# Optimization experiments

Measured on AMD Instinct MI355X. Metric: run time of the kernel, lower is better.

Reference implementation:

```python
import jax, jax.numpy as jnp
import numpy as np

B, H, D, SIZE, S = 32, 16, 64, 262144, 1024
GAMMA = 0.99

def setup_inputs() -> dict:
    key = jax.random.key(0)
    k1, k2, k3, k4 = jax.random.split(key, 4)
    return {
        "query": jax.random.normal(k1, (B, H, D), jnp.float32),
        "key_store": jax.random.normal(k2, (SIZE, H, D), jnp.float32),
        "value_store": jax.random.normal(k3, (SIZE, H, D), jnp.float32),
        "logit_store": 0.1 * jax.random.normal(k4, (SIZE, H), jnp.float32),
    }

def _sample_indices(logit_store, batch, rng):
    # torch softmax over dim=0 (batch*head rows) => per-row weights over s are
    # w[s] proportional to exp(logit[s,h]) / sum_h' exp(logit[s,h'])
    logw = logit_store.T - jax.nn.logsumexp(logit_store, axis=1)[None, :]  # (H, SIZE)
    u = jax.random.uniform(rng, (batch,) + logw.shape, minval=1e-12, maxval=1.0)
    gumbel = -jnp.log(-jnp.log(u))
    # Gumbel top-k == sampling without replacement proportional to exp(logw)
    _, idx = jax.lax.top_k(logw[None] + gumbel, S)  # (B, H, S)
    return idx

def reference(query, key_store, value_store, logit_store):
    b, h, d = query.shape
    idx = _sample_indices(logit_store, b, jax.random.key(42))  # (B,H,S)
    hidx = jnp.arange(h)[None, :, None]  # (1,H,1) broadcasts against idx
    kst = key_store.transpose(1, 0, 2)   # (H, SIZE, D)
    vst = value_store.transpose(1, 0, 2)
    sk = kst[hidx, idx]  # (B,H,S,D) gathered sample keys
    sv = vst[hidx, idx]  # (B,H,S,D) gathered sample values
    attn = jax.nn.softmax(jnp.einsum('bhd,bhsd->bhs', query, sk) * (d ** -0.5), axis=-1)
    lerp_k = jnp.einsum('bhs,bhsd->bhd', attn, sk)
    lerp_v = jnp.einsum('bhs,bhsd->bhd', attn, sv)
    # scattered in-place store updates
    new_k = (1.0 - attn)[..., None] * sk + attn[..., None] * lerp_k[:, :, None, :]
    new_v = (1.0 - attn)[..., None] * sv + attn[..., None] * lerp_v[:, :, None, :]
    key_store_new = kst.at[hidx, idx].set(new_k).transpose(1, 0, 2)
    value_store_new = vst.at[hidx, idx].set(new_v).transpose(1, 0, 2)
    lst = logit_store.T  # (H, SIZE)
    new_l = GAMMA * lst[hidx, idx] + attn  # RHS uses gathered old logits (matches torch)
    logit_store_new = lst.at[hidx, idx].set(new_l).T
    return lerp_k, lerp_v, key_store_new, value_store_new, logit_store_new
```

## Files before the change

### kernel.cpp

```cpp
#include <hip/hip_runtime.h>
#include <stdint.h>

static constexpr int NB = 32, NH = 16, ND = 64, NS = 1024;
static constexpr int SZ = 262144;
static constexpr int NROW = NB * NH;
static constexpr long N4 = 67108864L;
static constexpr long SPLIT4 = 50331648L;
static constexpr int SPLIT_IDX = 196608;

typedef float f32x4 __attribute__((ext_vector_type(4)));

__device__ __forceinline__ uint32_t rotl32(uint32_t x, int r) { return (x << r) | (x >> (32 - r)); }

__device__ __forceinline__ void tf2x32(uint32_t x0, uint32_t x1, uint32_t& o0, uint32_t& o1) {
  const uint32_t K1 = 42u, K2 = 0x1BD11BF0u;
  x1 += K1;
#define TFR(r) { x0 += x1; x1 = rotl32(x1, (r)); x1 ^= x0; }
  TFR(13) TFR(15) TFR(26) TFR(6)
  x0 += K1; x1 += K2 + 1u;
  TFR(17) TFR(29) TFR(16) TFR(24)
  x0 += K2; x1 += 2u;
  TFR(13) TFR(15) TFR(26) TFR(6)
  x1 += K1 + 3u;
  TFR(17) TFR(29) TFR(16) TFR(24)
  x0 += K1; x1 += K2 + 4u;
  TFR(13) TFR(15) TFR(26) TFR(6)
  x0 += K2; x1 += 5u;
#undef TFR
  o0 = x0; o1 = x1;
}

__device__ __forceinline__ uint32_t bits_of(uint32_t row, uint32_t s) {
  uint32_t o0, o1; tf2x32(0u, (row << 18) | s, o0, o1);
  return o0 ^ o1;
}

__device__ __forceinline__ float gumbel_precise(uint32_t row, uint32_t s) {
  uint32_t bits = bits_of(row, s);
  float f = __uint_as_float((bits >> 9) | 0x3f800000u) - 1.0f;
  float u = fmaxf(1e-12f, f + 1e-12f);
  float t = -logf(u);
  return -logf(t);
}

__device__ __forceinline__ float uf_of(uint32_t row, uint32_t s) {
  return __uint_as_float((bits_of(row, s) >> 9) | 0x3f800000u);
}

__device__ __forceinline__ uint32_t fkey(float v) {
  uint32_t u = __float_as_uint(v);
  return (u & 0x80000000u) ? ~u : (u | 0x80000000u);
}

__global__ void k_logw(const float* __restrict__ logit, float* __restrict__ logw,
                       float* __restrict__ wexp, float* __restrict__ outL,
                       int* __restrict__ winner, float* __restrict__ W) {
  __shared__ float sW[16];
  const int tid = threadIdx.x;
  if (tid < 16) sW[tid] = 0.f;
  __syncthreads();
  int s = blockIdx.x * 256 + tid;
  const float4* p = (const float4*)(logit + (size_t)s * NH);
  float4 a0 = p[0], a1 = p[1], a2 = p[2], a3 = p[3];
  float x[16] = {a0.x,a0.y,a0.z,a0.w, a1.x,a1.y,a1.z,a1.w,
                 a2.x,a2.y,a2.z,a2.w, a3.x,a3.y,a3.z,a3.w};
  float m = x[0];
#pragma unroll
  for (int h = 1; h < 16; ++h) m = fmaxf(m, x[h]);
  float acc = 0.f;
#pragma unroll
  for (int h = 0; h < 16; ++h) acc += expf(x[h] - m);
  float lse = logf(acc) + m;
  float wl[16];
#pragma unroll
  for (int h = 0; h < 16; ++h) {
    float lw = x[h] - lse;
    logw[(size_t)h * SZ + s] = lw;
    float e = expf(lw);
    wexp[(size_t)h * SZ + s] = e;
    wl[h] = e;
  }
#pragma unroll
  for (int h = 0; h < 16; ++h) {
    float v = wl[h];
#pragma unroll
    for (int off = 32; off; off >>= 1) v += __shfl_xor(v, off);
    if ((tid & 63) == 0) atomicAdd(&sW[h], v);
  }
  float4* q = (float4*)(outL + (size_t)s * NH);
  q[0] = a0; q[1] = a1; q[2] = a2; q[3] = a3;
  int4 mone = make_int4(-1, -1, -1, -1);
  int4* w = (int4*)(winner + (size_t)s * NH);
  w[0] = mone; w[1] = mone; w[2] = mone; w[3] = mone;
  __syncthreads();
  if (tid < 16) atomicAdd(&W[tid], sW[tid]);
}

__device__ __forceinline__ void find_thresh(const uint32_t* hist, int nbins, int chunk,
                                            uint32_t need, int* outT, int tid) {
  if (tid < 64) {
    int hi = nbins - 1 - tid * chunk;
    uint32_t csum = 0;
    for (int j = 0; j < chunk; ++j) csum += hist[hi - j];
    uint32_t inc = csum;
#pragma unroll
    for (int off = 1; off < 64; off <<= 1) {
      uint32_t t = (uint32_t)__shfl_up((int)inc, off);
      if (tid >= off) inc += t;
    }
    uint32_t pre = inc - csum;
    if (pre < need && inc >= need) {
      uint32_t cum = pre; int T = hi - chunk + 1;
      for (int j = 0; j < chunk; ++j) {
        int b = hi - j;
        if (cum + hist[b] >= need) { T = b; break; }
        cum += hist[b];
      }
      *outT = T;
    }
  }
}

#define MEGA_T 512
#define SEL_BLKS 512
#define COPY_BLKS 2048
#define NCAND 5120
__global__ void __launch_bounds__(MEGA_T, 8) k_mega(
    const float* __restrict__ logw, const float* __restrict__ wexp,
    const float* __restrict__ Wsum, const float* __restrict__ qin,
    const float* __restrict__ Kst, const float* __restrict__ Vst,
    int* __restrict__ idx_sel, float* __restrict__ attn_ws,
    float* __restrict__ lerp_k, float* __restrict__ lerp_v, int* __restrict__ winner,
    f32x4* __restrict__ oK4, f32x4* __restrict__ oV4) {
  const int bid = blockIdx.x;
  const int tid = threadIdx.x;

  if (bid >= SEL_BLKS) {
    const f32x4* K4 = (const f32x4*)Kst;
    const f32x4* V4 = (const f32x4*)Vst;
    const long base = (long)(bid - SEL_BLKS) * MEGA_T + tid;
    const long stride = (long)COPY_BLKS * MEGA_T;
    for (int r = 0; r < 12; ++r) {
      long i0 = base + (long)(4 * r) * stride;
      long i1 = i0 + stride, i2 = i0 + 2 * stride, i3 = i0 + 3 * stride;
      f32x4 k0 = __builtin_nontemporal_load(&K4[i0]);
      f32x4 k1 = __builtin_nontemporal_load(&K4[i1]);
      f32x4 k2 = __builtin_nontemporal_load(&K4[i2]);
      f32x4 k3 = __builtin_nontemporal_load(&K4[i3]);
      f32x4 v0 = __builtin_nontemporal_load(&V4[i0]);
      f32x4 v1 = __builtin_nontemporal_load(&V4[i1]);
      f32x4 v2 = __builtin_nontemporal_load(&V4[i2]);
      f32x4 v3 = __builtin_nontemporal_load(&V4[i3]);
      __builtin_nontemporal_store(k0, &oK4[i0]);
      __builtin_nontemporal_store(k1, &oK4[i1]);
      __builtin_nontemporal_store(k2, &oK4[i2]);
      __builtin_nontemporal_store(k3, &oK4[i3]);
      __builtin_nontemporal_store(v0, &oV4[i0]);
      __builtin_nontemporal_store(v1, &oV4[i1]);
      __builtin_nontemporal_store(v2, &oV4[i2]);
      __builtin_nontemporal_store(v3, &oV4[i3]);
    }
    return;
  }

  const int row = bid;
  const int h = row & 15, b = row >> 4;
  const float* lw = logw + (size_t)h * SZ;
  const f32x4* we4 = (const f32x4*)(wexp + (size_t)h * SZ);
  int* outrow = idx_sel + (size_t)row * NS;

  __shared__ union {
    struct {
      int      cidx[NCAND];
      uint32_t hist[2048];
      uint16_t candA[2048];
      uint16_t candB[256];
      uint16_t candC[64];
    } s;
    struct {
      int   sel_s[NS];
      float sc[NS];
      float red[MEGA_T];
      f32x4 pk4[8][16], pv4[8][16];
    } a;
  } u;
  __shared__ int ctl[8];
  __shared__ float sNB;

  if (tid == 0) {
    float Wh = Wsum[h];
    sNB = -4096.0f / Wh;
    ctl[1] = 0;
  }
  __syncthreads();
  const float nB = sNB;
  const float CThr = 1.9999996f;

  for (int g = tid; g < SZ / 4; g += MEGA_T) {
    f32x4 w4 = we4[g];
    int s0 = g << 2;
    float u0 = uf_of(row, s0);
    float u1 = uf_of(row, s0 + 1);
    float u2 = uf_of(row, s0 + 2);
    float u3 = uf_of(row, s0 + 3);
    if (u0 >= fmaf(nB, w4.x, CThr)) { int p = atomicAdd(&ctl[1], 1); if (p < NCAND) u.s.cidx[p] = s0; }
    if (u1 >= fmaf(nB, w4.y, CThr)) { int p = atomicAdd(&ctl[1], 1); if (p < NCAND) u.s.cidx[p] = s0 + 1; }
    if (u2 >= fmaf(nB, w4.z, CThr)) { int p = atomicAdd(&ctl[1], 1); if (p < NCAND) u.s.cidx[p] = s0 + 2; }
    if (u3 >= fmaf(nB, w4.w, CThr)) { int p = atomicAdd(&ctl[1], 1); if (p < NCAND) u.s.cidx[p] = s0 + 3; }
  }
  __syncthreads();
  const int C = min(ctl[1], NCAND);

  for (int i = tid; i < 2048; i += MEGA_T) u.s.hist[i] = 0;
  if (tid == 0) { ctl[0] = 0; ctl[3] = 0; ctl[4] = 0; ctl[5] = 0; }
  __syncthreads();
  for (int ci = tid; ci < C; ci += MEGA_T) {
    int s = u.s.cidx[ci];
    uint32_t k = fkey(lw[s] + gumbel_precise(row, s));
    atomicAdd(&u.s.hist[k >> 21], 1u);
  }
  __syncthreads();
  find_thresh(u.s.hist, 2048, 32, (uint32_t)NS, &ctl[2], tid);
  __syncthreads();
  const int T0 = ctl[2];
  for (int ci = tid; ci < C; ci += MEGA_T) {
    int s = u.s.cidx[ci];
    uint32_t k = fkey(lw[s] + gumbel_precise(row, s));
    int bb = (int)(k >> 21);
    if (bb > T0)       { int p = atomicAdd(&ctl[0], 1); outrow[p] = s; }
    else if (bb == T0) { int c = atomicAdd(&ctl[3], 1); if (c < 2048) u.s.candA[c] = (uint16_t)ci; }
  }
  __syncthreads();
  const int CA = min(ctl[3], 2048);
  for (int i = tid; i < 2048; i += MEGA_T) u.s.hist[i] = 0;
  __syncthreads();
  for (int i = tid; i < CA; i += MEGA_T) {
    int s = u.s.cidx[u.s.candA[i]];
    uint32_t k = fkey(lw[s] + gumbel_precise(row, s));
    atomicAdd(&u.s.hist[(k >> 10) & 0x7FFu], 1u);
  }
  __syncthreads();
  find_thresh(u.s.hist, 2048, 32, (uint32_t)(NS - ctl[0]), &ctl[2], tid);
  __syncthreads();
  const int T1 = ctl[2];
  for (int i = tid; i < CA; i += MEGA_T) {
    int ci = u.s.candA[i];
    int s = u.s.cidx[ci];
    uint32_t k = fkey(lw[s] + gumbel_precise(row, s));
    int mid = (int)((k >> 10) & 0x7FFu);
    if (mid > T1)       { int p = atomicAdd(&ctl[0], 1); outrow[p] = s; }
    else if (mid == T1) { int c = atomicAdd(&ctl[4], 1); if (c < 256) u.s.candB[c] = (uint16_t)ci; }
  }
  __syncthreads();
  const int CB = min(ctl[4], 256);
  for (int i = tid; i < 1024; i += MEGA_T) u.s.hist[i] = 0;
  __syncthreads();
  for (int i = tid; i < CB; i += MEGA_T) {
    int s = u.s.cidx[u.s.candB[i]];
    uint32_t k = fkey(lw[s] + gumbel_precise(row, s));
    atomicAdd(&u.s.hist[k & 0x3FFu], 1u);
  }
  __syncthreads();
  find_thresh(u.s.hist, 1024, 16, (uint32_t)(NS - ctl[0]), &ctl[2], tid);
  __syncthreads();
  const int T2 = ctl[2];
  for (int i = tid; i < CB; i += MEGA_T) {
    int ci = u.s.candB[i];
    int s = u.s.cidx[ci];
    uint32_t k = fkey(lw[s] + gumbel_precise(row, s));
    int lo = (int)(k & 0x3FFu);
    if (lo > T2)       { int p = atomicAdd(&ctl[0], 1); outrow[p] = s; }
    else if (lo == T2) { int c = atomicAdd(&ctl[5], 1); if (c < 64) u.s.candC[c] = (uint16_t)ci; }
  }
  __syncthreads();
  if (tid == 0) {
    int need = NS - ctl[0];
    int cc = min(ctl[5], 64);
    for (int k = 0; k < need; ++k) {
      int best = 0x7fffffff, bi = 0;
      for (int j = 0; j < cc; ++j) { int s = u.s.cidx[u.s.candC[j]]; if (s < best) { best = s; bi = j; } }
      if (best == 0x7fffffff) best = 0;
      outrow[ctl[0] + k] = best;
      if (cc > 0) u.s.cidx[u.s.candC[bi]] = 0x7fffffff;
    }
  }
  __syncthreads();

  const f32x4* K4 = (const f32x4*)Kst;
  const f32x4* V4 = (const f32x4*)Vst;
  const int lane = tid & 63, wv = tid >> 6;
  const int sj = lane >> 3, dj = lane & 7;
  for (int i = tid; i < NS; i += MEGA_T) u.a.sel_s[i] = outrow[i];
  const f32x4* q4 = (const f32x4*)(qin + (size_t)row * ND);
  f32x4 qa = q4[dj * 2], qb = q4[dj * 2 + 1];
  __syncthreads();
  for (int it = 0; it < 16; it += 2) {
    int i1 = it * 64 + wv * 8 + sj;
    int i2 = i1 + 64;
    int x1 = u.a.sel_s[i1], x2 = u.a.sel_s[i2];
    size_t b1 = ((size_t)x1 * NH + h) * 16 + dj * 2;
    size_t b2 = ((size_t)x2 * NH + h) * 16 + dj * 2;
    f32x4 ka1 = K4[b1], kb1 = K4[b1 + 1];
    f32x4 ka2 = K4[b2], kb2 = K4[b2 + 1];
    float p1 = ka1.x*qa.x + ka1.y*qa.y + ka1.z*qa.z + ka1.w*qa.w
             + kb1.x*qb.x + kb1.y*qb.y + kb1.z*qb.z + kb1.w*qb.w;
    float p2 = ka2.x*qa.x + ka2.y*qa.y + ka2.z*qa.z + ka2.w*qa.w
             + kb2.x*qb.x + kb2.y*qb.y + kb2.z*qb.z + kb2.w*qb.w;
#pragma unroll
    for (int off = 1; off < 8; off <<= 1) { p1 += __shfl_xor(p1, off); p2 += __shfl_xor(p2, off); }
    if (dj == 0) { u.a.sc[i1] = p1 * 0.125f; u.a.sc[i2] = p2 * 0.125f; }
  }
  __syncthreads();
  float v1 = u.a.sc[tid], v2 = u.a.sc[tid + 512];
  u.a.red[tid] = fmaxf(v1, v2); __syncthreads();
  for (int s = 256; s; s >>= 1) { if (tid < s) u.a.red[tid] = fmaxf(u.a.red[tid], u.a.red[tid + s]); __syncthreads(); }
  float m = u.a.red[0]; __syncthreads();
  float e1 = expf(v1 - m), e2 = expf(v2 - m);
  u.a.red[tid] = e1 + e2; __syncthreads();
  for (int s = 256; s; s >>= 1) { if (tid < s) u.a.red[tid] += u.a.red[tid + s]; __syncthreads(); }
  float inv = 1.0f / u.a.red[0];
  float a1 = e1 * inv, a2 = e2 * inv;
  u.a.sc[tid] = a1; u.a.sc[tid + 512] = a2;
  attn_ws[(size_t)row * NS + tid] = a1;
  attn_ws[(size_t)row * NS + tid + 512] = a2;
  __syncthreads();
  f32x4 AK = 0.f, BK = 0.f, AV = 0.f, BV = 0.f;
  for (int it = 0; it < 16; it += 2) {
    int i1 = it * 64 + wv * 8 + sj;
    int i2 = i1 + 64;
    int x1 = u.a.sel_s[i1], x2 = u.a.sel_s[i2];
    float c1 = u.a.sc[i1], c2 = u.a.sc[i2];
    size_t b1 = ((size_t)x1 * NH + h) * 16 + dj * 2;
    size_t b2 = ((size_t)x2 * NH + h) * 16 + dj * 2;
    f32x4 k1a = K4[b1], k1b = K4[b1 + 1], v1a = V4[b1], v1b = V4[b1 + 1];
    f32x4 k2a = K4[b2], k2b = K4[b2 + 1], v2a = V4[b2], v2b = V4[b2 + 1];
    AK += c1 * k1a + c2 * k2a; BK += c1 * k1b + c2 * k2b;
    AV += c1 * v1a + c2 * v2a; BV += c1 * v1b + c2 * v2b;
  }
#pragma unroll
  for (int off = 8; off < 64; off <<= 1) {
    AK.x += __shfl_xor(AK.x, off); AK.y += __shfl_xor(AK.y, off);
    AK.z += __shfl_xor(AK.z, off); AK.w += __shfl_xor(AK.w, off);
    BK.x += __shfl_xor(BK.x, off); BK.y += __shfl_xor(BK.y, off);
    BK.z += __shfl_xor(BK.z, off); BK.w += __shfl_xor(BK.w, off);
    AV.x += __shfl_xor(AV.x, off); AV.y += __shfl_xor(AV.y, off);
    AV.z += __shfl_xor(AV.z, off); AV.w += __shfl_xor(AV.w, off);
    BV.x += __shfl_xor(BV.x, off); BV.y += __shfl_xor(BV.y, off);
    BV.w += __shfl_xor(BV.w, off); BV.z += __shfl_xor(BV.z, off);
  }
  if (sj == 0) {
    u.a.pk4[wv][dj * 2] = AK; u.a.pk4[wv][dj * 2 + 1] = BK;
    u.a.pv4[wv][dj * 2] = AV; u.a.pv4[wv][dj * 2 + 1] = BV;
  }
  __syncthreads();
  if (tid < 64) {
    float lk = 0.f, lv = 0.f;
    const float* pkf = (const float*)u.a.pk4;
    const float* pvf = (const float*)u.a.pv4;
#pragma unroll
    for (int ww = 0; ww < 8; ++ww) { lk += pkf[ww * 64 + tid]; lv += pvf[ww * 64 + tid]; }
    lerp_k[(size_t)row * ND + tid] = lk;
    lerp_v[(size_t)row * ND + tid] = lv;
  }
  for (int i = tid; i < NS; i += MEGA_T) atomicMax(&winner[(size_t)u.a.sel_s[i] * NH + h], b);
}

__global__ void k_mark(const int* __restrict__ idx_sel, const float* __restrict__ attn_ws,
                       const int* __restrict__ winner, const float* __restrict__ Lst,
                       float* __restrict__ wa, float* __restrict__ outL) {
  int t = blockIdx.x * 256 + threadIdx.x;
  int row = t >> 10, h = row & 15, b = row >> 4;
  int idx = idx_sel[t];
  size_t slot = (size_t)idx * NH + h;
  if (winner[slot] == b) {
    float a = attn_ws[t];
    wa[slot] = a;
    outL[slot] = 0.99f * Lst[slot] + a;
  }
}

__global__ void __launch_bounds__(512) k_emit2(const f32x4* __restrict__ K4,
    const f32x4* __restrict__ V4, const int* __restrict__ winner,
    const float* __restrict__ wa, const f32x4* __restrict__ LK4,
    const f32x4* __restrict__ LV4, f32x4* __restrict__ oK4, f32x4* __restrict__ oV4) {
  const long base = SPLIT4 + (long)blockIdx.x * 512 + threadIdx.x;
  const long stride = 2048L * 512;
  for (int r = 0; r < 4; ++r) {
    long i0 = base + (long)(4 * r) * stride;
    long i1 = i0 + stride, i2 = i0 + 2 * stride, i3 = i0 + 3 * stride;
    int s0 = (int)(i0 >> 4), s1 = (int)(i1 >> 4), s2 = (int)(i2 >> 4), s3 = (int)(i3 >> 4);
    int w0 = winner[s0], w1 = winner[s1], w2 = winner[s2], w3 = winner[s3];
    f32x4 k0 = __builtin_nontemporal_load(&K4[i0]);
    f32x4 k1 = __builtin_nontemporal_load(&K4[i1]);
    f32x4 k2 = __builtin_nontemporal_load(&K4[i2]);
    f32x4 k3 = __builtin_nontemporal_load(&K4[i3]);
    f32x4 v0 = __builtin_nontemporal_load(&V4[i0]);
    f32x4 v1 = __builtin_nontemporal_load(&V4[i1]);
    f32x4 v2 = __builtin_nontemporal_load(&V4[i2]);
    f32x4 v3 = __builtin_nontemporal_load(&V4[i3]);
    if (w0 >= 0) {
      float a = wa[s0]; int rr = (w0 << 4) | (s0 & 15); float o = 1.0f - a;
      k0 = o * k0 + a * LK4[((long)rr << 4) + (i0 & 15)];
      v0 = o * v0 + a * LV4[((long)rr << 4) + (i0 & 15)];
    }
    if (w1 >= 0) {
      float a = wa[s1]; int rr = (w1 << 4) | (s1 & 15); float o = 1.0f - a;
      k1 = o * k1 + a * LK4[((long)rr << 4) + (i1 & 15)];
      v1 = o * v1 + a * LV4[((long)rr << 4) + (i1 & 15)];
    }
    if (w2 >= 0) {
      float a = wa[s2]; int rr = (w2 << 4) | (s2 & 15); float o = 1.0f - a;
      k2 = o * k2 + a * LK4[((long)rr << 4) + (i2 & 15)];
      v2 = o * v2 + a * LV4[((long)rr << 4) + (i2 & 15)];
    }
    if (w3 >= 0) {
      float a = wa[s3]; int rr = (w3 << 4) | (s3 & 15); float o = 1.0f - a;
      k3 = o * k3 + a * LK4[((long)rr << 4) + (i3 & 15)];
      v3 = o * v3 + a * LV4[((long)rr << 4) + (i3 & 15)];
    }
    __builtin_nontemporal_store(k0, &oK4[i0]);
    __builtin_nontemporal_store(k1, &oK4[i1]);
    __builtin_nontemporal_store(k2, &oK4[i2]);
    __builtin_nontemporal_store(k3, &oK4[i3]);
    __builtin_nontemporal_store(v0, &oV4[i0]);
    __builtin_nontemporal_store(v1, &oV4[i1]);
    __builtin_nontemporal_store(v2, &oV4[i2]);
    __builtin_nontemporal_store(v3, &oV4[i3]);
  }
}

__global__ void __launch_bounds__(256) k_fixup(const float* __restrict__ Kst,
    const float* __restrict__ Vst, const int* __restrict__ idx_sel,
    const float* __restrict__ attn_ws, const int* __restrict__ winner,
    const float* __restrict__ lerp_k, const float* __restrict__ lerp_v,
    float* __restrict__ outK, float* __restrict__ outV) {
  int g = blockIdx.x * 4 + (threadIdx.x >> 6);
  int lane = threadIdx.x & 63;
  int row = g >> 10, i = g & 1023;
  int h = row & 15, b = row >> 4;
  int idx = idx_sel[(size_t)row * NS + i];
  if (idx >= SPLIT_IDX) return;
  size_t slot = (size_t)idx * NH + h;
  if (winner[slot] != b) return;
  float a = attn_ws[(size_t)row * NS + i];
  size_t base = slot * ND + lane;
  float kv = Kst[base], vv = Vst[base];
  float lk = lerp_k[(size_t)row * ND + lane], lv = lerp_v[(size_t)row * ND + lane];
  float o = 1.0f - a;
  outK[base] = o * kv + a * lk;
  outV[base] = o * vv + a * lv;
}

extern "C" void kernel_launch(void* const* d_in, const int* in_sizes, int n_in,
                              void* d_out, int out_size, void* d_ws, size_t ws_size,
                              hipStream_t stream) {
  const float* q   = (const float*)d_in[0];
  const float* Kst = (const float*)d_in[1];
  const float* Vst = (const float*)d_in[2];
  const float* Lst = (const float*)d_in[3];

  float* out    = (float*)d_out;
  float* out_lk = out;
  float* out_lv = out + 32768;
  float* outK   = out + 65536;
  float* outV   = outK + 268435456;
  float* outL   = outV + 268435456;

  char* ws = (char*)d_ws;
  float* logw   = (float*)ws;
  float* wexp   = (float*)(ws + (16ull << 20));
  int*   idxsel = (int*)(ws + (32ull << 20));
  float* attn   = (float*)(ws + (34ull << 20));
  int*   winner = (int*)(ws + (36ull << 20));
  float* wa     = (float*)(ws + (52ull << 20));
  float* Wsum   = (float*)(ws + (68ull << 20));

  hipMemsetAsync(Wsum, 0, 16 * sizeof(float), stream);
  k_logw<<<SZ / 256, 256, 0, stream>>>(Lst, logw, wexp, outL, winner, Wsum);
  k_mega<<<SEL_BLKS + COPY_BLKS, MEGA_T, 0, stream>>>(logw, wexp, Wsum, q, Kst, Vst,
                                                      idxsel, attn, out_lk, out_lv, winner,
                                                      (f32x4*)outK, (f32x4*)outV);
  k_mark<<<NROW * NS / 256, 256, 0, stream>>>(idxsel, attn, winner, Lst, wa, outL);
  k_emit2<<<2048, 512, 0, stream>>>((const f32x4*)Kst, (const f32x4*)Vst, winner, wa,
                                    (const f32x4*)out_lk, (const f32x4*)out_lv,
                                    (f32x4*)outK, (f32x4*)outV);
  k_fixup<<<NROW * NS / 4, 256, 0, stream>>>(Kst, Vst, idxsel, attn, winner,
                                             out_lk, out_lv, outK, outV);
}
```

Baseline: 1.173 ms.

## Split store copy evenly and fuse emit and fixup into one tail kernel

```diff
diff --git a/kernel.cpp b/kernel.cpp
--- a/kernel.cpp
+++ b/kernel.cpp
@@ -5,8 +5,8 @@
 static constexpr int SZ = 262144;
 static constexpr int NROW = NB * NH;
 static constexpr long N4 = 67108864L;
-static constexpr long SPLIT4 = 50331648L;
-static constexpr int SPLIT_IDX = 196608;
+static constexpr long HALF4 = 33554432L;
+static constexpr int SPLIT_IDX = 131072;
 
 typedef float f32x4 __attribute__((ext_vector_type(4)));
 
@@ -140,7 +140,7 @@
     const f32x4* V4 = (const f32x4*)Vst;
     const long base = (long)(bid - SEL_BLKS) * MEGA_T + tid;
     const long stride = (long)COPY_BLKS * MEGA_T;
-    for (int r = 0; r < 12; ++r) {
+    for (int r = 0; r < 8; ++r) {
       long i0 = base + (long)(4 * r) * stride;
       long i1 = i0 + stride, i2 = i0 + 2 * stride, i3 = i0 + 3 * stride;
       f32x4 k0 = __builtin_nontemporal_load(&K4[i0]);
@@ -346,7 +346,7 @@
     AV.x += __shfl_xor(AV.x, off); AV.y += __shfl_xor(AV.y, off);
     AV.z += __shfl_xor(AV.z, off); AV.w += __shfl_xor(AV.w, off);
     BV.x += __shfl_xor(BV.x, off); BV.y += __shfl_xor(BV.y, off);
-    BV.w += __shfl_xor(BV.w, off); BV.z += __shfl_xor(BV.z, off);
+    BV.z += __shfl_xor(BV.z, off); BV.w += __shfl_xor(BV.w, off);
   }
   if (sj == 0) {
     u.a.pk4[wv][dj * 2] = AK; u.a.pk4[wv][dj * 2 + 1] = BK;
@@ -379,62 +379,61 @@
   }
 }
 
-__global__ void __launch_bounds__(512) k_emit2(const f32x4* __restrict__ K4,
+#define TAIL_COPY_BLKS 4096
+__global__ void __launch_bounds__(256) k_tail(const f32x4* __restrict__ K4,
     const f32x4* __restrict__ V4, const int* __restrict__ winner,
     const float* __restrict__ wa, const f32x4* __restrict__ LK4,
-    const f32x4* __restrict__ LV4, f32x4* __restrict__ oK4, f32x4* __restrict__ oV4) {
-  const long base = SPLIT4 + (long)blockIdx.x * 512 + threadIdx.x;
-  const long stride = 2048L * 512;
-  for (int r = 0; r < 4; ++r) {
-    long i0 = base + (long)(4 * r) * stride;
-    long i1 = i0 + stride, i2 = i0 + 2 * stride, i3 = i0 + 3 * stride;
-    int s0 = (int)(i0 >> 4), s1 = (int)(i1 >> 4), s2 = (int)(i2 >> 4), s3 = (int)(i3 >> 4);
-    int w0 = winner[s0], w1 = winner[s1], w2 = winner[s2], w3 = winner[s3];
-    f32x4 k0 = __builtin_nontemporal_load(&K4[i0]);
-    f32x4 k1 = __builtin_nontemporal_load(&K4[i1]);
-    f32x4 k2 = __builtin_nontemporal_load(&K4[i2]);
-    f32x4 k3 = __builtin_nontemporal_load(&K4[i3]);
-    f32x4 v0 = __builtin_nontemporal_load(&V4[i0]);
-    f32x4 v1 = __builtin_nontemporal_load(&V4[i1]);
-    f32x4 v2 = __builtin_nontemporal_load(&V4[i2]);
-    f32x4 v3 = __builtin_nontemporal_load(&V4[i3]);
-    if (w0 >= 0) {
-      float a = wa[s0]; int rr = (w0 << 4) | (s0 & 15); float o = 1.0f - a;
-      k0 = o * k0 + a * LK4[((long)rr << 4) + (i0 & 15)];
-      v0 = o * v0 + a * LV4[((long)rr << 4) + (i0 & 15)];
+    const f32x4* __restrict__ LV4, const int* __restrict__ idx_sel,
+    const float* __restrict__ attn_ws, f32x4* __restrict__ oK4, f32x4* __restrict__ oV4) {
+  const int bid = blockIdx.x;
+  if (bid < TAIL_COPY_BLKS) {
+    const long base = HALF4 + (long)bid * 256 + threadIdx.x;
+    const long stride = (long)TAIL_COPY_BLKS * 256;
+    for (int r = 0; r < 8; ++r) {
+      long i0 = base + (long)(4 * r) * stride;
+      long i1 = i0 + stride, i2 = i0 + 2 * stride, i3 = i0 + 3 * stride;
+      int s0 = (int)(i0 >> 4), s1 = (int)(i1 >> 4), s2 = (int)(i2 >> 4), s3 = (int)(i3 >> 4);
+      int w0 = winner[s0], w1 = winner[s1], w2 = winner[s2], w3 = winner[s3];
+      f32x4 k0 = __builtin_nontemporal_load(&K4[i0]);
+      f32x4 k1 = __builtin_nontemporal_load(&K4[i1]);
+      f32x4 k2 = __builtin_nontemporal_load(&K4[i2]);
+      f32x4 k3 = __builtin_nontemporal_load(&K4[i3]);
+      f32x4 v0 = __builtin_nontemporal_load(&V4[i0]);
+      f32x4 v1 = __builtin_nontemporal_load(&V4[i1]);
+      f32x4 v2 = __builtin_nontemporal_load(&V4[i2]);
+      f32x4 v3 = __builtin_nontemporal_load(&V4[i3]);
+      if (w0 >= 0) {
+        float a = wa[s0]; int rr = (w0 << 4) | (s0 & 15); float o = 1.0f - a;
+        k0 = o * k0 + a * LK4[((long)rr << 4) + (i0 & 15)];
+        v0 = o * v0 + a * LV4[((long)rr << 4) + (i0 & 15)];
+      }
+      if (w1 >= 0) {
+        float a = wa[s1]; int rr = (w1 << 4) | (s1 & 15); float o = 1.0f - a;
+        k1 = o * k1 + a * LK4[((long)rr << 4) + (i1 & 15)];
+        v1 = o * v1 + a * LV4[((long)rr << 4) + (i1 & 15)];
+      }
+      if (w2 >= 0) {
+        float a = wa[s2]; int rr = (w2 << 4) | (s2 & 15); float o = 1.0f - a;
+        k2 = o * k2 + a * LK4[((long)rr << 4) + (i2 & 15)];
+        v2 = o * v2 + a * LV4[((long)rr << 4) + (i2 & 15)];
+      }
+      if (w3 >= 0) {
+        float a = wa[s3]; int rr = (w3 << 4) | (s3 & 15); float o = 1.0f - a;
+        k3 = o * k3 + a * LK4[((long)rr << 4) + (i3 & 15)];
+        v3 = o * v3 + a * LV4[((long)rr << 4) + (i3 & 15)];
+      }
+      __builtin_nontemporal_store(k0, &oK4[i0]);
+      __builtin_nontemporal_store(k1, &oK4[i1]);
+      __builtin_nontemporal_store(k2, &oK4[i2]);
+      __builtin_nontemporal_store(k3, &oK4[i3]);
+      __builtin_nontemporal_store(v0, &oV4[i0]);
+      __builtin_nontemporal_store(v1, &oV4[i1]);
+      __builtin_nontemporal_store(v2, &oV4[i2]);
+      __builtin_nontemporal_store(v3, &oV4[i3]);
     }
-    if (w1 >= 0) {
-      float a = wa[s1]; int rr = (w1 << 4) | (s1 & 15); float o = 1.0f - a;
-      k1 = o * k1 + a * LK4[((long)rr << 4) + (i1 & 15)];
-      v1 = o * v1 + a * LV4[((long)rr << 4) + (i1 & 15)];
-    }
-    if (w2 >= 0) {
-      float a = wa[s2]; int rr = (w2 << 4) | (s2 & 15); float o = 1.0f - a;
-      k2 = o * k2 + a * LK4[((long)rr << 4) + (i2 & 15)];
-      v2 = o * v2 + a * LV4[((long)rr << 4) + (i2 & 15)];
-    }
-    if (w3 >= 0) {
-      float a = wa[s3]; int rr = (w3 << 4) | (s3 & 15); float o = 1.0f - a;
-      k3 = o * k3 + a * LK4[((long)rr << 4) + (i3 & 15)];
-      v3 = o * v3 + a * LV4[((long)rr << 4) + (i3 & 15)];
-    }
-    __builtin_nontemporal_store(k0, &oK4[i0]);
-    __builtin_nontemporal_store(k1, &oK4[i1]);
-    __builtin_nontemporal_store(k2, &oK4[i2]);
-    __builtin_nontemporal_store(k3, &oK4[i3]);
-    __builtin_nontemporal_store(v0, &oV4[i0]);
-    __builtin_nontemporal_store(v1, &oV4[i1]);
-    __builtin_nontemporal_store(v2, &oV4[i2]);
-    __builtin_nontemporal_store(v3, &oV4[i3]);
-  }
-}
-
-__global__ void __launch_bounds__(256) k_fixup(const float* __restrict__ Kst,
-    const float* __restrict__ Vst, const int* __restrict__ idx_sel,
-    const float* __restrict__ attn_ws, const int* __restrict__ winner,
-    const float* __restrict__ lerp_k, const float* __restrict__ lerp_v,
-    float* __restrict__ outK, float* __restrict__ outV) {
-  int g = blockIdx.x * 4 + (threadIdx.x >> 6);
+    return;
+  }
+  int g = (bid - TAIL_COPY_BLKS) * 4 + (threadIdx.x >> 6);
   int lane = threadIdx.x & 63;
   int row = g >> 10, i = g & 1023;
   int h = row & 15, b = row >> 4;
@@ -443,12 +442,13 @@
   size_t slot = (size_t)idx * NH + h;
   if (winner[slot] != b) return;
   float a = attn_ws[(size_t)row * NS + i];
-  size_t base = slot * ND + lane;
-  float kv = Kst[base], vv = Vst[base];
-  float lk = lerp_k[(size_t)row * ND + lane], lv = lerp_v[(size_t)row * ND + lane];
+  size_t base = slot * (size_t)ND + lane;
+  float kv = ((const float*)K4)[base], vv = ((const float*)V4)[base];
+  float lk = ((const float*)LK4)[(size_t)row * ND + lane];
+  float lv = ((const float*)LV4)[(size_t)row * ND + lane];
   float o = 1.0f - a;
-  outK[base] = o * kv + a * lk;
-  outV[base] = o * vv + a * lv;
+  ((float*)oK4)[base] = o * kv + a * lk;
+  ((float*)oV4)[base] = o * vv + a * lv;
 }
 
 extern "C" void kernel_launch(void* const* d_in, const int* in_sizes, int n_in,
@@ -481,9 +481,8 @@
                                                       idxsel, attn, out_lk, out_lv, winner,
                                                       (f32x4*)outK, (f32x4*)outV);
   k_mark<<<NROW * NS / 256, 256, 0, stream>>>(idxsel, attn, winner, Lst, wa, outL);
-  k_emit2<<<2048, 512, 0, stream>>>((const f32x4*)Kst, (const f32x4*)Vst, winner, wa,
-                                    (const f32x4*)out_lk, (const f32x4*)out_lv,
-                                    (f32x4*)outK, (f32x4*)outV);
-  k_fixup<<<NROW * NS / 4, 256, 0, stream>>>(Kst, Vst, idxsel, attn, winner,
-                                             out_lk, out_lv, outK, outV);
-}
+  k_tail<<<TAIL_COPY_BLKS + NROW * NS / 4, 256, 0, stream>>>(
+      (const f32x4*)Kst, (const f32x4*)Vst, winner, wa,
+      (const f32x4*)out_lk, (const f32x4*)out_lv, idxsel, attn,
+      (f32x4*)outK, (f32x4*)outV);
+}
```

Measured after the change: 1.172 ms. No clear change (-0.1%).
